# Kernel tuning notes

Measured on AMD Instinct MI355X. Metric: run time of the kernel, lower is better.

The kernel has to match this reference:

```python
import jax, jax.numpy as jnp
import numpy as np

EMBED_DIM = 1024
NUM_HEADS = 16
HEAD_DIM = EMBED_DIM // NUM_HEADS
SCALE = HEAD_DIM ** -0.5
B, S = 2, 2048


def setup_inputs() -> dict:
    key = jax.random.key(0)
    ks = jax.random.split(key, 11)
    lim = 1.0 / np.sqrt(EMBED_DIM)
    def lin(kw, kb):
        W = jax.random.uniform(kw, (EMBED_DIM, EMBED_DIM), jnp.float32, -lim, lim)
        b = jax.random.uniform(kb, (EMBED_DIM,), jnp.float32, -lim, lim)
        return W, b
    Wq, bq = lin(ks[0], ks[1])
    Wk, bk = lin(ks[2], ks[3])
    Wv, bv = lin(ks[4], ks[5])
    Wo, bo = lin(ks[6], ks[7])
    query = jax.random.normal(ks[8], (B, S, EMBED_DIM), jnp.float32)
    key_t = jax.random.normal(ks[9], (B, S, EMBED_DIM), jnp.float32)
    value = jax.random.normal(ks[10], (B, S, EMBED_DIM), jnp.float32)
    return {"query": query, "key": key_t, "value": value,
            "Wq": Wq, "bq": bq, "Wk": Wk, "bk": bk,
            "Wv": Wv, "bv": bv, "Wo": Wo, "bo": bo}


def reference(query, key, value, Wq, bq, Wk, bk, Wv, bv, Wo, bo):
    # 'flash' path with attn_mask=None == full softmax attention (chunking is
    # only an execution schedule; per-chunk softmax is over the full key axis).
    b, s, _ = query.shape
    def heads(x, W, bias):
        y = x @ W.T + bias                      # [b, s, E]
        return y.reshape(b, s, NUM_HEADS, HEAD_DIM).transpose(0, 2, 1, 3)  # [b, h, s, d]
    q = heads(query, Wq, bq)
    k = heads(key, Wk, bk)
    v = heads(value, Wv, bv)
    scores = jnp.einsum('bhqd,bhkd->bhqk', q, k) * SCALE
    attn = jax.nn.softmax(scores, axis=-1)
    out = jnp.einsum('bhqk,bhkd->bhqd', attn, v)
    out = out.transpose(0, 2, 1, 3).reshape(b, s, EMBED_DIM)
    return out @ Wo.T + bo
```

## Files before the change

### kernel.cpp

```cpp
#include <hip/hip_runtime.h>

typedef unsigned short u16;
typedef unsigned int u32;
typedef __attribute__((ext_vector_type(8))) __bf16 bf16x8;
typedef __attribute__((ext_vector_type(4))) float f32x4;
typedef __attribute__((ext_vector_type(4))) unsigned short u16x4;
typedef __attribute__((ext_vector_type(8))) unsigned short u16x8;
typedef __attribute__((ext_vector_type(2))) unsigned int u32x2;
typedef __attribute__((ext_vector_type(4))) unsigned int u32x4;

#define DEV static __device__ __forceinline__

DEV void async_copy16(const void* g, void* l) {
  __builtin_amdgcn_global_load_lds((const __attribute__((address_space(1))) void*)g,
                                   (__attribute__((address_space(3))) void*)l, 16, 0, 0);
}
DEV float b2f(u16 s) { union { unsigned u; float f; } v; v.u = ((unsigned)s) << 16; return v.f; }
DEV u16 f2b(float f) {
  union { float f; unsigned u; } v; v.f = f;
  unsigned r = v.u + 0x7FFFu + ((v.u >> 16) & 1u);
  return (u16)(r >> 16);
}
DEV u32 pack2bf(float a, float b) {
  u32 ua = __float_as_uint(a) + 0x8000u;
  u32 ub = __float_as_uint(b) + 0x8000u;
  return __builtin_amdgcn_perm(ub, ua, 0x07060302u);
}

#define MFMA(a, b, c) __builtin_amdgcn_mfma_f32_16x16x32_bf16((a), (b), (c), 0, 0, 0)

__global__ void detect_dtype(const unsigned* __restrict__ q, int* __restrict__ flag) {
  const int lane = threadIdx.x;
  const unsigned w = q[lane];
  const unsigned e = (w >> 7) & 0xFFu;
  const bool inr = (e >= 100u && e <= 132u);
  const unsigned long long m = __ballot(inr);
  if (lane == 0) flag[0] = (__popcll(m) >= 48) ? 1 : 0;
}

__global__ void convert_inputs(
    const void* s0, const void* s1, const void* s2,
    const void* s3, const void* s4, const void* s5, const void* s6,
    const void* s7, const void* s8, const void* s9, const void* s10,
    u16* __restrict__ d0, u16* __restrict__ d1, u16* __restrict__ d2,
    u16* __restrict__ d3, u16* __restrict__ d4, u16* __restrict__ d5, u16* __restrict__ d6,
    float* __restrict__ e7, float* __restrict__ e8, float* __restrict__ e9, float* __restrict__ e10,
    const int* __restrict__ flag)
{
  const int bi = blockIdx.y;
  const void* src = nullptr; u16* db = nullptr; float* df = nullptr; int n = 0;
  switch (bi) {
    case 0:  src = s0;  db = d0; n = 4194304; break;
    case 1:  src = s1;  db = d1; n = 4194304; break;
    case 2:  src = s2;  db = d2; n = 4194304; break;
    case 3:  src = s3;  db = d3; n = 1048576; break;
    case 4:  src = s4;  db = d4; n = 1048576; break;
    case 5:  src = s5;  db = d5; n = 1048576; break;
    case 6:  src = s6;  db = d6; n = 1048576; break;
    case 7:  src = s7;  df = e7; n = 1024; break;
    case 8:  src = s8;  df = e8; n = 1024; break;
    case 9:  src = s9;  df = e9; n = 1024; break;
    default: src = s10; df = e10; n = 1024; break;
  }
  const int isbf = flag[0];
  const int stride = gridDim.x * 256 * 8;
  for (int i = (blockIdx.x * 256 + threadIdx.x) * 8; i < n; i += stride) {
    if (db) {
      u16x8 v;
      if (isbf) {
        v = *(const u16x8*)((const u16*)src + i);
      } else {
        const float* sf = (const float*)src;
#pragma unroll
        for (int j = 0; j < 8; ++j) v[j] = f2b(sf[i + j]);
      }
      *(u16x8*)(db + i) = v;
    } else {
#pragma unroll
      for (int j = 0; j < 8; ++j) {
        float x = isbf ? b2f(((const u16*)src)[i + j]) : ((const float*)src)[i + j];
        df[i + j] = x;
      }
    }
  }
}

__global__ void gemm_qkv(const u16* __restrict__ X0, const u16* __restrict__ X1, const u16* __restrict__ X2,
                         const u16* __restrict__ W0, const u16* __restrict__ W1, const u16* __restrict__ W2,
                         const float* __restrict__ B0, const float* __restrict__ B1, const float* __restrict__ B2,
                         u16* __restrict__ Y0, u16* __restrict__ Y1, u16* __restrict__ Y2,
                         float* __restrict__ Yf, const int* __restrict__ flag, int mode0)
{
  __shared__ __align__(16) u16 smem[17408];

  const int z = blockIdx.z;
  const u16* X  = (z == 0) ? X0 : ((z == 1) ? X1 : X2);
  const u16* W  = (z == 0) ? W0 : ((z == 1) ? W1 : W2);
  const float* Bi = (z == 0) ? B0 : ((z == 1) ? B1 : B2);
  u16* Y        = (z == 0) ? Y0 : ((z == 1) ? Y1 : Y2);
  const int mode = mode0 ? mode0 : z;
  const int outbf = flag[0];

  const int t = threadIdx.x, wave = t >> 6, lane = t & 63;
  const int lane15 = lane & 15, quad = lane >> 4;

  const int L = blockIdx.y * 8 + blockIdx.x;
  const int wrk = (L & 7) * 32 + (L >> 3);
  const int m0 = (wrk >> 3) * 128, n0 = (wrk & 7) * 128;

  const u16* gA = X + (size_t)(m0 + wave * 16 + (lane >> 2)) * 1024 + (lane & 3) * 8;
  const u16* gB = W + (size_t)(n0 + wave * 16 + (lane >> 2)) * 1024 + (lane & 3) * 8;

  f32x4 acc[4][4];
#pragma unroll
  for (int i = 0; i < 4; ++i)
#pragma unroll
    for (int j = 0; j < 4; ++j) acc[i][j] = (f32x4){0.f, 0.f, 0.f, 0.f};

  const int wr = wave >> 1, wc = wave & 1;

  u16* lA0 = smem + wave * 512;
  u16* lB0 = smem + 4096 + wave * 512;
  u16* lA1 = smem + 8192 + wave * 512;
  u16* lB1 = smem + 12288 + wave * 512;

  auto stage = [&](u16* lA, u16* lB) {
    async_copy16(gA, lA);
    async_copy16(gA + 64 * 1024, lA + 64 * 32);
    async_copy16(gB, lB);
    async_copy16(gB + 64 * 1024, lB + 64 * 32);
    gA += 32; gB += 32;
  };
  auto compute = [&](const u16* As_, const u16* Bs_) {
    bf16x8 af[4], bfv[4];
#pragma unroll
    for (int mt = 0; mt < 4; ++mt)
      af[mt] = *(const bf16x8*)&As_[(wr * 64 + mt * 16 + lane15) * 32 + quad * 8];
#pragma unroll
    for (int nt = 0; nt < 4; ++nt)
      bfv[nt] = *(const bf16x8*)&Bs_[(wc * 64 + nt * 16 + lane15) * 32 + quad * 8];
    __builtin_amdgcn_s_setprio(1);
#pragma unroll
    for (int mt = 0; mt < 4; ++mt)
#pragma unroll
      for (int nt = 0; nt < 4; ++nt)
        acc[mt][nt] = MFMA(af[mt], bfv[nt], acc[mt][nt]);
    __builtin_amdgcn_s_setprio(0);
  };

  stage(lA0, lB0);
  __syncthreads();

  for (int k0 = 0; k0 < 1024; k0 += 64) {
    if (k0 + 32 < 1024) stage(lA1, lB1);
    compute(smem, smem + 4096);
    __syncthreads();
    if (k0 + 64 < 1024) stage(lA0, lB0);
    compute(smem + 8192, smem + 12288);
    __syncthreads();
  }

  const float qscale = 0.125f * 1.44269504088896340736f;

  if (mode == 2) {
    u16* T2 = smem;
#pragma unroll
    for (int mt = 0; mt < 4; ++mt) {
      const int sl_base = wr * 64 + mt * 16 + quad * 4;
#pragma unroll
      for (int nt = 0; nt < 4; ++nt) {
        const int nn = wc * 64 + nt * 16 + lane15;
        const float bias_v = Bi[n0 + nn];
#pragma unroll
        for (int r = 0; r < 4; ++r) {
          const int sl = sl_base + r;
          const int r5 = sl & 31;
          const int p = (((r5 >> 2) & 3) << 3) | (((r5 >> 4) & 1) << 2) | (r5 & 3);
          T2[nn * 136 + (sl & ~31) + p] = f2b(acc[mt][nt][r] + bias_v);
        }
      }
    }
    __syncthreads();
    const size_t grow0 = (size_t)(m0 >> 11) * 1024 + n0;
    const int col0 = m0 & 2047;
#pragma unroll
    for (int i = 0; i < 8; ++i) {
      const int id = i * 256 + t;
      const int row = id >> 4, ch = id & 15;
      *(u16x8*)&Y[(grow0 + row) * 2048 + col0 + ch * 8] = *(const u16x8*)&T2[row * 136 + ch * 8];
    }
    return;
  }

#pragma unroll
  for (int mt = 0; mt < 4; ++mt) {
    const int m_base = m0 + wr * 64 + mt * 16 + quad * 4;
#pragma unroll
    for (int nt = 0; nt < 4; ++nt) {
      const int n = n0 + wc * 64 + nt * 16 + lane15;
      const float bias_v = Bi[n];
#pragma unroll
      for (int r = 0; r < 4; ++r) {
        const int m = m_base + r;
        float v = acc[mt][nt][r] + bias_v;
        if (mode == 0) v *= qscale;
        if (mode == 3) {
          if (outbf) Y[(size_t)m * 1024 + n] = f2b(v);
          else       Yf[(size_t)m * 1024 + n] = v;
        } else {
          size_t addr = (((size_t)(m >> 11) * 16 + (n >> 6)) * 2048 + (size_t)(m & 2047)) * 64 + (n & 63);
          Y[addr] = f2b(v);
        }
      }
    }
  }
}

__global__ __launch_bounds__(256, 4) void flash_attn(const u16* __restrict__ Qs, const u16* __restrict__ Ks,
                                                     const u16* __restrict__ Vt, u16* __restrict__ AO)
{
  __shared__ __align__(16) u16 smem[16384];
  u16* Kt = smem;
  u16* Vs = smem + 8192;

  const int t = threadIdx.x, wave = t >> 6, lane = t & 63;
  const int lane15 = lane & 15, quad = lane >> 4;
  const int l7 = lane15 & 7;
  const int h = wave >> 1;
  const int c = wave & 1;

  const int Lb = blockIdx.y * 16 + blockIdx.x;
  const int wrk = (Lb & 7) * 128 + (Lb >> 3);
  const int bh = wrk >> 5;
  const int q0 = (wrk & 31) * 64;

  const u16* Qb = Qs + ((size_t)bh * 2048 + q0) * 64;
  const u16* Kb = Ks + (size_t)bh * 2048 * 64;
  const u16* Vb = Vt + (size_t)bh * 64 * 2048;

  const int krow = lane >> 3;
  const int kchunk = (lane & 7) ^ (krow & 7);
  const int vrow = lane >> 4;
  const int vchunk = (lane & 15) ^ (((wave & 1) << 2) + vrow);

#pragma unroll
  for (int r = 0; r < 2; ++r)
    async_copy16(Qb + (size_t)(r * 32 + wave * 8 + krow) * 64 + kchunk * 8,
                 &Kt[(r * 32 + wave * 8) * 64]);
  __syncthreads();
  bf16x8 aq[2][2];
#pragma unroll
  for (int mt = 0; mt < 2; ++mt)
#pragma unroll
    for (int ks = 0; ks < 2; ++ks)
      aq[mt][ks] = *(const bf16x8*)&Kt[(h * 32 + mt * 16 + lane15) * 64 + ((ks * 4 + quad) ^ l7) * 8];
  __syncthreads();

  f32x4 acc_o[2][4];
  f32x4 acc_l[2];
#pragma unroll
  for (int mt = 0; mt < 2; ++mt) {
    acc_l[mt] = (f32x4){0.f, 0.f, 0.f, 0.f};
#pragma unroll
    for (int i = 0; i < 4; ++i) acc_o[mt][i] = (f32x4){0.f, 0.f, 0.f, 0.f};
  }

  u16x8 ou;
#pragma unroll
  for (int j = 0; j < 8; ++j) ou[j] = 0x3F80;
  const bf16x8 ones = __builtin_bit_cast(bf16x8, ou);

  for (int kt = 0; kt < 16; ++kt) {
#pragma unroll
    for (int r = 0; r < 4; ++r)
      async_copy16(Kb + (size_t)(kt * 128 + r * 32 + wave * 8 + krow) * 64 + kchunk * 8,
                   &Kt[(r * 32 + wave * 8) * 64]);
#pragma unroll
    for (int r = 0; r < 4; ++r)
      async_copy16(Vb + (size_t)(r * 16 + wave * 4 + vrow) * 2048 + kt * 128 + vchunk * 8,
                   &Vs[(r * 16 + wave * 4) * 128]);
    __syncthreads();

#pragma unroll
    for (int g = 0; g < 2; ++g) {
      const int ks2 = c * 2 + g;
      bf16x8 bk[2][2];
#pragma unroll
      for (int no = 0; no < 2; ++no)
#pragma unroll
        for (int ks = 0; ks < 2; ++ks)
          bk[no][ks] = *(const bf16x8*)&Kt[(c * 64 + g * 32 + no * 16 + lane15) * 64 + ((ks * 4 + quad) ^ l7) * 8];

      bf16x8 pa[2];
#pragma unroll
      for (int mt = 0; mt < 2; ++mt) {
        f32x4 s2[2];
        s2[0] = (f32x4){0.f, 0.f, 0.f, 0.f};
        s2[1] = (f32x4){0.f, 0.f, 0.f, 0.f};
        __builtin_amdgcn_s_setprio(1);
#pragma unroll
        for (int no = 0; no < 2; ++no)
#pragma unroll
          for (int ks = 0; ks < 2; ++ks)
            s2[no] = MFMA(bk[no][ks], aq[mt][ks], s2[no]);
        __builtin_amdgcn_s_setprio(0);

        float e0[4], e1[4];
#pragma unroll
        for (int rg = 0; rg < 4; ++rg) {
          e0[rg] = __builtin_amdgcn_exp2f(s2[0][rg]);
          e1[rg] = __builtin_amdgcn_exp2f(s2[1][rg]);
        }
        const u32x4 paw = (u32x4){pack2bf(e0[0], e0[1]), pack2bf(e0[2], e0[3]),
                                  pack2bf(e1[0], e1[1]), pack2bf(e1[2], e1[3])};
        pa[mt] = __builtin_bit_cast(bf16x8, paw);
      }

      bf16x8 bv[4];
#pragma unroll
      for (int dt = 0; dt < 4; ++dt)
        bv[dt] = *(const bf16x8*)&Vs[(dt * 16 + lane15) * 128 + ((ks2 * 4 + quad) ^ l7) * 8];
      __builtin_amdgcn_s_setprio(1);
#pragma unroll
      for (int mt = 0; mt < 2; ++mt) {
#pragma unroll
        for (int dt = 0; dt < 4; ++dt)
          acc_o[mt][dt] = MFMA(pa[mt], bv[dt], acc_o[mt][dt]);
        acc_l[mt] = MFMA(pa[mt], ones, acc_l[mt]);
      }
      __builtin_amdgcn_s_setprio(0);
    }
    __syncthreads();
  }

  float* Of = (float*)smem;
  if (c == 1) {
#pragma unroll
    for (int mt = 0; mt < 2; ++mt)
#pragma unroll
      for (int dt = 0; dt < 4; ++dt)
#pragma unroll
        for (int rg = 0; rg < 4; ++rg)
          Of[h * 2048 + (mt * 16 + quad * 4 + rg) * 64 + dt * 16 + lane15] = acc_o[mt][dt][rg];
  }
  __syncthreads();
  if (c == 0) {
#pragma unroll
    for (int mt = 0; mt < 2; ++mt)
#pragma unroll
      for (int dt = 0; dt < 4; ++dt)
#pragma unroll
        for (int rg = 0; rg < 4; ++rg)
          acc_o[mt][dt][rg] += Of[h * 2048 + (mt * 16 + quad * 4 + rg) * 64 + dt * 16 + lane15];
  }
  __syncthreads();
  float* Lf = (float*)smem;
  if (c == 1 && lane15 == 0) {
#pragma unroll
    for (int mt = 0; mt < 2; ++mt)
#pragma unroll
      for (int rg = 0; rg < 4; ++rg)
        Lf[h * 32 + mt * 16 + quad * 4 + rg] = acc_l[mt][rg];
  }
  __syncthreads();
  float rinv[2][4];
  if (c == 0) {
#pragma unroll
    for (int mt = 0; mt < 2; ++mt)
#pragma unroll
      for (int rg = 0; rg < 4; ++rg)
        rinv[mt][rg] = 1.0f / (acc_l[mt][rg] + Lf[h * 32 + mt * 16 + quad * 4 + rg]);
  }
  __syncthreads();

  u16* T = smem;
  if (c == 0) {
#pragma unroll
    for (int mt = 0; mt < 2; ++mt)
#pragma unroll
      for (int dt = 0; dt < 4; ++dt)
#pragma unroll
        for (int rg = 0; rg < 4; ++rg)
          T[(h * 32 + mt * 16 + quad * 4 + rg) * 72 + dt * 16 + lane15] =
              f2b(acc_o[mt][dt][rg] * rinv[mt][rg]);
  }
  __syncthreads();

  const int b = bh >> 4, hh = bh & 15;
#pragma unroll
  for (int i = 0; i < 2; ++i) {
    const int id = i * 256 + t;
    const int row = id >> 3, ch = id & 7;
    *(u16x8*)&AO[((size_t)b * 2048 + q0 + row) * 1024 + hh * 64 + ch * 8] =
        *(const u16x8*)&T[row * 72 + ch * 8];
  }
}

extern "C" void kernel_launch(void* const* d_in, const int* in_sizes, int n_in,
                              void* d_out, int out_size, void* d_ws, size_t ws_size,
                              hipStream_t stream)
{
  const void* query = d_in[0];
  const void* key_  = d_in[1];
  const void* value = d_in[2];
  const void* Wq = d_in[3]; const void* bq = d_in[4];
  const void* Wk = d_in[5]; const void* bk = d_in[6];
  const void* Wv = d_in[7]; const void* bv = d_in[8];
  const void* Wo = d_in[9]; const void* bo = d_in[10];

  u16* ws = (u16*)d_ws;
  u16* Qs  = ws;
  u16* Ks  = Qs + 4194304;
  u16* Vt  = Ks + 4194304;
  u16* AO  = Vt + 4194304;
  u16* Xq  = AO + 4194304;
  u16* Xk  = Xq + 4194304;
  u16* Xv  = Xk + 4194304;
  u16* Wqc = Xv + 4194304;
  u16* Wkc = Wqc + 1048576;
  u16* Wvc = Wkc + 1048576;
  u16* Woc = Wvc + 1048576;
  float* Bc = (float*)(Woc + 1048576);
  int* flag = (int*)(Bc + 4096);

  detect_dtype<<<1, 64, 0, stream>>>((const unsigned*)query, flag);
  convert_inputs<<<dim3(128, 11), 256, 0, stream>>>(
      query, key_, value, Wq, Wk, Wv, Wo, bq, bk, bv, bo,
      Xq, Xk, Xv, Wqc, Wkc, Wvc, Woc,
      Bc, Bc + 1024, Bc + 2048, Bc + 3072, flag);

  gemm_qkv<<<dim3(8, 32, 3), 256, 0, stream>>>(Xq, Xk, Xv, Wqc, Wkc, Wvc,
                                               Bc, Bc + 1024, Bc + 2048,
                                               Qs, Ks, Vt, nullptr, flag, 0);
  flash_attn<<<dim3(16, 64), 256, 0, stream>>>(Qs, Ks, Vt, AO);
  gemm_qkv<<<dim3(8, 32, 1), 256, 0, stream>>>(AO, AO, AO, Woc, Woc, Woc,
                                               Bc + 3072, Bc + 3072, Bc + 3072,
                                               (u16*)d_out, (u16*)d_out, (u16*)d_out,
                                               (float*)d_out, flag, 3);
}
```

Before: 216.7 us.

## Fuse fp32 activation conversion into QKV GEMM load path and drop detect kernel

The separate pass that converted the query, key and value activations to bf16 is removed. The QKV GEMM now reads fp32 activations directly with register loads, rounds them to bf16 and writes them into LDS, while weights still use async global-to-LDS copies. The dtype-detection kernel is replaced by an inline ballot probe in each kernel, so one launch goes away and the 48 MB of activation conversion traffic is avoided. In exchange the GEMM A-operand path becomes synchronous register staging, which may expose load latency, and the kernel gains a launch bound of 3 that limits registers.

```diff
diff --git a/kernel.cpp b/kernel.cpp
--- a/kernel.cpp
+++ b/kernel.cpp
@@ -26,43 +26,42 @@
   u32 ub = __float_as_uint(b) + 0x8000u;
   return __builtin_amdgcn_perm(ub, ua, 0x07060302u);
 }
-
-#define MFMA(a, b, c) __builtin_amdgcn_mfma_f32_16x16x32_bf16((a), (b), (c), 0, 0, 0)
-
-__global__ void detect_dtype(const unsigned* __restrict__ q, int* __restrict__ flag) {
-  const int lane = threadIdx.x;
-  const unsigned w = q[lane];
-  const unsigned e = (w >> 7) & 0xFFu;
+DEV u32 pack2bf_rne(float a, float b) {
+  u32 ua = __float_as_uint(a); ua += 0x7FFFu + ((ua >> 16) & 1u);
+  u32 ub = __float_as_uint(b); ub += 0x7FFFu + ((ub >> 16) & 1u);
+  return __builtin_amdgcn_perm(ub, ua, 0x07060302u);
+}
+DEV int probe_isbf(const u32* __restrict__ q, int lane) {
+  const u32 w = q[lane & 63];
+  const u32 e = (w >> 7) & 0xFFu;
   const bool inr = (e >= 100u && e <= 132u);
   const unsigned long long m = __ballot(inr);
-  if (lane == 0) flag[0] = (__popcll(m) >= 48) ? 1 : 0;
-}
-
-__global__ void convert_inputs(
-    const void* s0, const void* s1, const void* s2,
-    const void* s3, const void* s4, const void* s5, const void* s6,
-    const void* s7, const void* s8, const void* s9, const void* s10,
-    u16* __restrict__ d0, u16* __restrict__ d1, u16* __restrict__ d2,
-    u16* __restrict__ d3, u16* __restrict__ d4, u16* __restrict__ d5, u16* __restrict__ d6,
-    float* __restrict__ e7, float* __restrict__ e8, float* __restrict__ e9, float* __restrict__ e10,
-    const int* __restrict__ flag)
+  return (__popcll(m) >= 48) ? 1 : 0;
+}
+
+#define MFMA(a, b, c) __builtin_amdgcn_mfma_f32_16x16x32_bf16((a), (b), (c), 0, 0, 0)
+
+__global__ void convert_wb(const void* s0, const void* s1, const void* s2, const void* s3,
+                           const void* s4, const void* s5, const void* s6, const void* s7,
+                           u16* __restrict__ d0, u16* __restrict__ d1,
+                           u16* __restrict__ d2, u16* __restrict__ d3,
+                           float* __restrict__ e4, float* __restrict__ e5,
+                           float* __restrict__ e6, float* __restrict__ e7,
+                           const u32* __restrict__ det)
 {
   const int bi = blockIdx.y;
   const void* src = nullptr; u16* db = nullptr; float* df = nullptr; int n = 0;
   switch (bi) {
-    case 0:  src = s0;  db = d0; n = 4194304; break;
-    case 1:  src = s1;  db = d1; n = 4194304; break;
-    case 2:  src = s2;  db = d2; n = 4194304; break;
-    case 3:  src = s3;  db = d3; n = 1048576; break;
-    case 4:  src = s4;  db = d4; n = 1048576; break;
-    case 5:  src = s5;  db = d5; n = 1048576; break;
-    case 6:  src = s6;  db = d6; n = 1048576; break;
-    case 7:  src = s7;  df = e7; n = 1024; break;
-    case 8:  src = s8;  df = e8; n = 1024; break;
-    case 9:  src = s9;  df = e9; n = 1024; break;
-    default: src = s10; df = e10; n = 1024; break;
-  }
-  const int isbf = flag[0];
+    case 0:  src = s0; db = d0; n = 1048576; break;
+    case 1:  src = s1; db = d1; n = 1048576; break;
+    case 2:  src = s2; db = d2; n = 1048576; break;
+    case 3:  src = s3; db = d3; n = 1048576; break;
+    case 4:  src = s4; df = e4; n = 1024; break;
+    case 5:  src = s5; df = e5; n = 1024; break;
+    case 6:  src = s6; df = e6; n = 1024; break;
+    default: src = s7; df = e7; n = 1024; break;
+  }
+  const int isbf = probe_isbf(det, threadIdx.x & 63);
   const int stride = gridDim.x * 256 * 8;
   for (int i = (blockIdx.x * 256 + threadIdx.x) * 8; i < n; i += stride) {
     if (db) {
@@ -85,31 +84,37 @@
   }
 }
 
-__global__ void gemm_qkv(const u16* __restrict__ X0, const u16* __restrict__ X1, const u16* __restrict__ X2,
-                         const u16* __restrict__ W0, const u16* __restrict__ W1, const u16* __restrict__ W2,
-                         const float* __restrict__ B0, const float* __restrict__ B1, const float* __restrict__ B2,
-                         u16* __restrict__ Y0, u16* __restrict__ Y1, u16* __restrict__ Y2,
-                         float* __restrict__ Yf, const int* __restrict__ flag, int mode0)
+__global__ __launch_bounds__(256, 3) void gemm_qkv(
+    const void* __restrict__ X0, const void* __restrict__ X1, const void* __restrict__ X2,
+    const u16* __restrict__ W0, const u16* __restrict__ W1, const u16* __restrict__ W2,
+    const float* __restrict__ B0, const float* __restrict__ B1, const float* __restrict__ B2,
+    u16* __restrict__ Y0, u16* __restrict__ Y1, u16* __restrict__ Y2,
+    float* __restrict__ Yf, const u32* __restrict__ det, int mode0)
 {
   __shared__ __align__(16) u16 smem[17408];
 
   const int z = blockIdx.z;
-  const u16* X  = (z == 0) ? X0 : ((z == 1) ? X1 : X2);
-  const u16* W  = (z == 0) ? W0 : ((z == 1) ? W1 : W2);
+  const void* Xv = (z == 0) ? X0 : ((z == 1) ? X1 : X2);
+  const u16* W   = (z == 0) ? W0 : ((z == 1) ? W1 : W2);
   const float* Bi = (z == 0) ? B0 : ((z == 1) ? B1 : B2);
-  u16* Y        = (z == 0) ? Y0 : ((z == 1) ? Y1 : Y2);
+  u16* Y         = (z == 0) ? Y0 : ((z == 1) ? Y1 : Y2);
   const int mode = mode0 ? mode0 : z;
-  const int outbf = flag[0];
 
   const int t = threadIdx.x, wave = t >> 6, lane = t & 63;
   const int lane15 = lane & 15, quad = lane >> 4;
+
+  const int isbf = probe_isbf(det, lane);
+  const bool aF32 = (mode0 == 0) && !isbf;
 
   const int L = blockIdx.y * 8 + blockIdx.x;
   const int wrk = (L & 7) * 32 + (L >> 3);
   const int m0 = (wrk >> 3) * 128, n0 = (wrk & 7) * 128;
 
-  const u16* gA = X + (size_t)(m0 + wave * 16 + (lane >> 2)) * 1024 + (lane & 3) * 8;
-  const u16* gB = W + (size_t)(n0 + wave * 16 + (lane >> 2)) * 1024 + (lane & 3) * 8;
+  const size_t arow = (size_t)(m0 + wave * 16 + (lane >> 2)) * 1024 + (lane & 3) * 8;
+  const size_t brow = (size_t)(n0 + wave * 16 + (lane >> 2)) * 1024 + (lane & 3) * 8;
+  const u16* uA = (const u16*)Xv + arow;
+  const float* fA = (const float*)Xv + arow;
+  const u16* uB = W + brow;
 
   f32x4 acc[4][4];
 #pragma unroll
@@ -124,13 +129,31 @@
   u16* lA1 = smem + 8192 + wave * 512;
   u16* lB1 = smem + 12288 + wave * 512;
 
-  auto stage = [&](u16* lA, u16* lB) {
-    async_copy16(gA, lA);
-    async_copy16(gA + 64 * 1024, lA + 64 * 32);
-    async_copy16(gB, lB);
-    async_copy16(gB + 64 * 1024, lB + 64 * 32);
-    gA += 32; gB += 32;
+  auto stageA = [&](int k0, u16* lA) {
+    async_copy16(uA + k0, lA);
+    async_copy16(uA + k0 + 65536, lA + 2048);
   };
+  auto stageB = [&](int k0, u16* lB) {
+    async_copy16(uB + k0, lB);
+    async_copy16(uB + k0 + 65536, lB + 2048);
+  };
+
+  f32x4 pa0, pa1, pa2, pa3;
+  auto loadA = [&](int k0) {
+    pa0 = *(const f32x4*)(fA + k0);
+    pa1 = *(const f32x4*)(fA + k0 + 4);
+    pa2 = *(const f32x4*)(fA + k0 + 65536);
+    pa3 = *(const f32x4*)(fA + k0 + 65540);
+  };
+  auto writeA = [&](u16* lA) {
+    *(u32x4*)&lA[lane * 8] =
+        (u32x4){pack2bf_rne(pa0[0], pa0[1]), pack2bf_rne(pa0[2], pa0[3]),
+                pack2bf_rne(pa1[0], pa1[1]), pack2bf_rne(pa1[2], pa1[3])};
+    *(u32x4*)&lA[2048 + lane * 8] =
+        (u32x4){pack2bf_rne(pa2[0], pa2[1]), pack2bf_rne(pa2[2], pa2[3]),
+                pack2bf_rne(pa3[0], pa3[1]), pack2bf_rne(pa3[2], pa3[3])};
+  };
+
   auto compute = [&](const u16* As_, const u16* Bs_) {
     bf16x8 af[4], bfv[4];
 #pragma unroll
@@ -148,16 +171,35 @@
     __builtin_amdgcn_s_setprio(0);
   };
 
-  stage(lA0, lB0);
-  __syncthreads();
-
-  for (int k0 = 0; k0 < 1024; k0 += 64) {
-    if (k0 + 32 < 1024) stage(lA1, lB1);
-    compute(smem, smem + 4096);
+  if (aF32) {
+    loadA(0);
+    stageB(0, lB0);
+    writeA(lA0);
     __syncthreads();
-    if (k0 + 64 < 1024) stage(lA0, lB0);
-    compute(smem + 8192, smem + 12288);
+    for (int k0 = 0; k0 < 1024; k0 += 64) {
+      const bool p1 = (k0 + 32 < 1024), p2 = (k0 + 64 < 1024);
+      if (p1) { loadA(k0 + 32); stageB(k0 + 32, lB1); }
+      compute(smem, smem + 4096);
+      if (p1) writeA(lA1);
+      __syncthreads();
+      if (p2) { loadA(k0 + 64); stageB(k0 + 64, lB0); }
+      compute(smem + 8192, smem + 12288);
+      if (p2) writeA(lA0);
+      __syncthreads();
+    }
+  } else {
+    stageA(0, lA0);
+    stageB(0, lB0);
     __syncthreads();
+    for (int k0 = 0; k0 < 1024; k0 += 64) {
+      const bool p1 = (k0 + 32 < 1024), p2 = (k0 + 64 < 1024);
+      if (p1) { stageA(k0 + 32, lA1); stageB(k0 + 32, lB1); }
+      compute(smem, smem + 4096);
+      __syncthreads();
+      if (p2) { stageA(k0 + 64, lA0); stageB(k0 + 64, lB0); }
+      compute(smem + 8192, smem + 12288);
+      __syncthreads();
+    }
   }
 
   const float qscale = 0.125f * 1.44269504088896340736f;
@@ -205,8 +247,8 @@
         float v = acc[mt][nt][r] + bias_v;
         if (mode == 0) v *= qscale;
         if (mode == 3) {
-          if (outbf) Y[(size_t)m * 1024 + n] = f2b(v);
-          else       Yf[(size_t)m * 1024 + n] = v;
+          if (isbf) Y[(size_t)m * 1024 + n] = f2b(v);
+          else      Yf[(size_t)m * 1024 + n] = v;
         } else {
           size_t addr = (((size_t)(m >> 11) * 16 + (n >> 6)) * 2048 + (size_t)(m & 2047)) * 64 + (n & 63);
           Y[addr] = f2b(v);
@@ -413,28 +455,26 @@
   u16* Ks  = Qs + 4194304;
   u16* Vt  = Ks + 4194304;
   u16* AO  = Vt + 4194304;
-  u16* Xq  = AO + 4194304;
-  u16* Xk  = Xq + 4194304;
-  u16* Xv  = Xk + 4194304;
-  u16* Wqc = Xv + 4194304;
+  u16* Wqc = AO + 4194304;
   u16* Wkc = Wqc + 1048576;
   u16* Wvc = Wkc + 1048576;
   u16* Woc = Wvc + 1048576;
   float* Bc = (float*)(Woc + 1048576);
-  int* flag = (int*)(Bc + 4096);
-
-  detect_dtype<<<1, 64, 0, stream>>>((const unsigned*)query, flag);
-  convert_inputs<<<dim3(128, 11), 256, 0, stream>>>(
-      query, key_, value, Wq, Wk, Wv, Wo, bq, bk, bv, bo,
-      Xq, Xk, Xv, Wqc, Wkc, Wvc, Woc,
-      Bc, Bc + 1024, Bc + 2048, Bc + 3072, flag);
-
-  gemm_qkv<<<dim3(8, 32, 3), 256, 0, stream>>>(Xq, Xk, Xv, Wqc, Wkc, Wvc,
+
+  convert_wb<<<dim3(64, 8), 256, 0, stream>>>(
+      Wq, Wk, Wv, Wo, bq, bk, bv, bo,
+      Wqc, Wkc, Wvc, Woc,
+      Bc, Bc + 1024, Bc + 2048, Bc + 3072, (const u32*)query);
+
+  gemm_qkv<<<dim3(8, 32, 3), 256, 0, stream>>>(query, key_, value,
+                                               Wqc, Wkc, Wvc,
                                                Bc, Bc + 1024, Bc + 2048,
-                                               Qs, Ks, Vt, nullptr, flag, 0);
+                                               Qs, Ks, Vt, nullptr,
+                                               (const u32*)query, 0);
   flash_attn<<<dim3(16, 64), 256, 0, stream>>>(Qs, Ks, Vt, AO);
-  gemm_qkv<<<dim3(8, 32, 1), 256, 0, stream>>>(AO, AO, AO, Woc, Woc, Woc,
+  gemm_qkv<<<dim3(8, 32, 1), 256, 0, stream>>>(AO, AO, AO,
+                                               Woc, Woc, Woc,
                                                Bc + 3072, Bc + 3072, Bc + 3072,
                                                (u16*)d_out, (u16*)d_out, (u16*)d_out,
-                                               (float*)d_out, flag, 3);
-}
+                                               (float*)d_out, (const u32*)query, 3);
+}
```

After: 225.2 us. 3.9% more time.
